# Performance work log

Measured on AMD Instinct MI355X. Metric: run time of the kernel, lower is better.

The kernel has to match this reference:

```python
import jax, jax.numpy as jnp
import numpy as np

N_NODES = 50000
N_EDGES = 800000


def setup_inputs() -> dict:
    key = jax.random.key(0)
    ks = jax.random.split(key, 8)
    x = jax.random.normal(ks[0], (N_NODES, 128), dtype=jnp.float32)
    edge_index = jax.random.randint(ks[1], (2, N_EDGES), 0, N_NODES, dtype=jnp.int64)
    # GCNConv weights (PyG: x @ W then propagate, bias after aggregation)
    W1 = jax.random.normal(ks[2], (128, 256), dtype=jnp.float32) / np.sqrt(128)
    b1 = jnp.zeros((256,), dtype=jnp.float32)
    W2 = jax.random.normal(ks[3], (256, 128), dtype=jnp.float32) / np.sqrt(256)
    b2 = jnp.zeros((128,), dtype=jnp.float32)
    # projection head
    fcW1 = jax.random.normal(ks[4], (128, 128), dtype=jnp.float32) / np.sqrt(128)
    fcb1 = jnp.zeros((128,), dtype=jnp.float32)
    fcW2 = jax.random.normal(ks[5], (128, 128), dtype=jnp.float32) / np.sqrt(128)
    fcb2 = jnp.zeros((128,), dtype=jnp.float32)
    return {"x": x, "edge_index": edge_index, "W1": W1, "b1": b1,
            "W2": W2, "b2": b2, "fcW1": fcW1, "fcb1": fcb1,
            "fcW2": fcW2, "fcb2": fcb2}


def _gcn_conv(x, W, b, src, dst, dinv):
    # x' = D^-1/2 (A + I) D^-1/2 (x W) + b  (GCN with self-loops)
    xw = x @ W                                             # [N, C]
    coeff = dinv[src] * dinv[dst]                          # [E]
    msg = xw[src] * coeff[:, None]                         # [E, C] gather
    agg = jax.ops.segment_sum(msg, dst, num_segments=N_NODES)  # scatter-add
    self_term = xw * (dinv * dinv)[:, None]                # self-loop
    return agg + self_term + b


def reference(x, edge_index, W1, b1, W2, b2, fcW1, fcb1, fcW2, fcb2):
    src, dst = edge_index[0], edge_index[1]
    # degree of A + I (in-degree on dst, weight 1 each, +1 self-loop)
    deg = jax.ops.segment_sum(jnp.ones((N_EDGES,), jnp.float32), dst,
                              num_segments=N_NODES) + 1.0
    dinv = jax.lax.rsqrt(deg)
    # Encoder: GCNConv -> relu -> GCNConv -> relu
    h = jax.nn.relu(_gcn_conv(x, W1, b1, src, dst, dinv))
    z = jax.nn.relu(_gcn_conv(h, W2, b2, src, dst, dinv))
    # projection: Linear -> ELU -> Linear
    p = jax.nn.elu(z @ fcW1 + fcb1)
    return p @ fcW2 + fcb2
```

## Files before the change

### kernel.cpp

```cpp
#include <hip/hip_runtime.h>
#include <hip/hip_bf16.h>
#include <cstdint>

#define N_NODES 50000
#define N_EDGES 800000
#define C128 128
#define SCAN_BLOCKS ((N_NODES + 255) / 256)

typedef __attribute__((ext_vector_type(8))) short bf16x8;
typedef __attribute__((ext_vector_type(4))) float f32x4;
typedef unsigned int u32;
typedef unsigned short u16;

__device__ __forceinline__ bf16x8 pack_bf16x8(u32 a, u32 b, u32 c, u32 d) {
    union { u32 u[4]; bf16x8 v; } x;
    x.u[0] = a; x.u[1] = b; x.u[2] = c; x.u[3] = d;
    return x.v;
}

__device__ __forceinline__ bf16x8 as_bf16x8(uint4 v) {
    union { uint4 u; bf16x8 b; } x;
    x.u = v;
    return x.b;
}

__device__ __forceinline__ u32 rne_bf16(float x) {
    u32 u = __float_as_uint(x);
    return (u + 0x7FFFu + ((u >> 16) & 1u)) >> 16;
}

__device__ __forceinline__ void stage16(const u32* g, u32* lds) {
    __builtin_amdgcn_global_load_lds(
        (const __attribute__((address_space(1))) u32*)g,
        (__attribute__((address_space(3))) u32*)lds, 16, 0, 0);
}


__global__ void k_zero(int* __restrict__ a, int n) {
    int i = blockIdx.x * blockDim.x + threadIdx.x;
    if (i < n) a[i] = 0;
}

__global__ void k_copy(const int* __restrict__ src, int* __restrict__ dst, int n) {
    int i = blockIdx.x * blockDim.x + threadIdx.x;
    if (i < n) dst[i] = src[i];
}

__device__ __forceinline__ int clamp_node(int v) {
    return v < 0 ? 0 : (v >= N_NODES ? N_NODES - 1 : v);
}

__global__ void k_count(const int* __restrict__ ei, int* __restrict__ counts) {
    int e = blockIdx.x * blockDim.x + threadIdx.x;
    if (e < N_EDGES) {
        int dst = clamp_node(ei[N_EDGES + e]);
        atomicAdd(&counts[dst], 1);
    }
}

__global__ void k_dinv(const int* __restrict__ counts, float* __restrict__ dinv) {
    int i = blockIdx.x * blockDim.x + threadIdx.x;
    if (i < N_NODES) {
        dinv[i] = rsqrtf((float)counts[i] + 1.0f);
    }
}

__global__ __launch_bounds__(256) void k_xscale(const float* __restrict__ x,
                                                const float* __restrict__ dinv,
                                                u32* __restrict__ xs ) {
    int idx = blockIdx.x * 256 + threadIdx.x;
    if (idx < N_NODES * 32) {
        int node = idx >> 5;
        float di = dinv[node];
        float4 v = reinterpret_cast<const float4*>(x)[idx];
        u32 w0 = rne_bf16(v.x * di) | (rne_bf16(v.y * di) << 16);
        u32 w1 = rne_bf16(v.z * di) | (rne_bf16(v.w * di) << 16);
        reinterpret_cast<uint2*>(xs)[idx] = make_uint2(w0, w1);
    }
}

__global__ __launch_bounds__(256) void k_scan1(const int* __restrict__ counts,
                                               int* __restrict__ part,
                                               int* __restrict__ bsum) {
    __shared__ int s[256];
    const int tid = threadIdx.x;
    const int i = blockIdx.x * 256 + tid;
    int v = (i < N_NODES) ? counts[i] : 0;
    s[tid] = v;
    __syncthreads();
    for (int off = 1; off < 256; off <<= 1) {
        int t = (tid >= off) ? s[tid - off] : 0;
        __syncthreads();
        s[tid] += t;
        __syncthreads();
    }
    if (i < N_NODES) part[i] = s[tid];
    if (tid == 255) bsum[blockIdx.x] = s[255];
}

__global__ __launch_bounds__(256) void k_scan2(const int* __restrict__ bsum,
                                               int* __restrict__ boff) {
    __shared__ int s[256];
    const int tid = threadIdx.x;
    int v = (tid < SCAN_BLOCKS) ? bsum[tid] : 0;
    s[tid] = v;
    __syncthreads();
    for (int off = 1; off < 256; off <<= 1) {
        int t = (tid >= off) ? s[tid - off] : 0;
        __syncthreads();
        s[tid] += t;
        __syncthreads();
    }
    if (tid < SCAN_BLOCKS) boff[tid] = s[tid] - v;
}

__global__ __launch_bounds__(256) void k_scan3(const int* __restrict__ part,
                                               const int* __restrict__ counts,
                                               const int* __restrict__ boff,
                                               int* __restrict__ offsets) {
    const int i = blockIdx.x * 256 + threadIdx.x;
    if (i < N_NODES) offsets[i] = part[i] - counts[i] + boff[blockIdx.x];
    if (i == 0) offsets[N_NODES] = N_EDGES;
}

__global__ void k_fill(const int* __restrict__ ei, int* __restrict__ cursor,
                       u16* __restrict__ csr) {
    int e = blockIdx.x * blockDim.x + threadIdx.x;
    if (e < N_EDGES) {
        int src = clamp_node(ei[e]);
        int dst = clamp_node(ei[N_EDGES + e]);
        int slot = atomicAdd(&cursor[dst], 1);
        if (slot >= 0 && slot < N_EDGES) csr[slot] = (u16)src;
    }
}


__global__ __launch_bounds__(64) void k_prep(const float* __restrict__ W1,
                                             const float* __restrict__ W2,
                                             const float* __restrict__ fcW1,
                                             const float* __restrict__ fcW2,
                                             u32* __restrict__ ftab) {
    int bx = blockIdx.x;
    int s = bx >> 5, f = bx & 31;
    int kf = f >> 3, nf = f & 7;
    int l = threadIdx.x;
    const float* src; int ld, roff, coff;
    switch (s) {
        case 0:  src = W1;   ld = 256; roff = 0;   coff = 0;   break;
        case 1:  src = W1;   ld = 256; roff = 0;   coff = 128; break;
        case 2:  src = W2;   ld = 128; roff = 0;   coff = 0;   break;
        case 3:  src = W2;   ld = 128; roff = 128; coff = 0;   break;
        case 4:  src = fcW1; ld = 128; roff = 0;   coff = 0;   break;
        default: src = fcW2; ld = 128; roff = 0;   coff = 0;   break;
    }
    int col = coff + nf * 16 + (l & 15);
    int krow = roff + kf * 32 + (l >> 4) * 8;
    u32 hp[4];
#pragma unroll
    for (int p = 0; p < 4; ++p) {
        float a0 = src[(size_t)(krow + 2 * p) * ld + col];
        float a1 = src[(size_t)(krow + 2 * p + 1) * ld + col];
        hp[p] = rne_bf16(a0) | (rne_bf16(a1) << 16);
    }
    u32* dst = ftab + (size_t)s * 8192 + (size_t)f * 256;
    *reinterpret_cast<uint4*>(dst + 4 * l) = make_uint4(hp[0], hp[1], hp[2], hp[3]);
}


template <bool HAS_BIAS, bool RELU>
__global__ __launch_bounds__(256) void k_prop(const u32* __restrict__ xs,
                                              float* __restrict__ out,
                                              const float* __restrict__ dinv,
                                              const int* __restrict__ offsets,
                                              const u16* __restrict__ csr,
                                              const float* __restrict__ bias) {
    const int wave = threadIdx.x >> 6;
    const int lane = threadIdx.x & 63;
    const int half = lane >> 5;
    const int lc   = lane & 31;
    const int node = (blockIdx.x * 4 + wave) * 2 + half;
    if (node >= N_NODES) return;

    const uint2* __restrict__ xp = reinterpret_cast<const uint2*>(xs);
    const float di = dinv[node];

    uint2 sv = xp[(size_t)node * 32 + lc];
    float ax = __uint_as_float(sv.x << 16);
    float ay = __uint_as_float(sv.x & 0xFFFF0000u);
    float az = __uint_as_float(sv.y << 16);
    float aw = __uint_as_float(sv.y & 0xFFFF0000u);

    int e = offsets[node];
    const int eend = offsets[node + 1];
    for (; e + 4 <= eend; e += 4) {
        int s0 = csr[e + 0], s1 = csr[e + 1], s2 = csr[e + 2], s3 = csr[e + 3];
        uint2 v0 = xp[(size_t)s0 * 32 + lc];
        uint2 v1 = xp[(size_t)s1 * 32 + lc];
        uint2 v2 = xp[(size_t)s2 * 32 + lc];
        uint2 v3 = xp[(size_t)s3 * 32 + lc];
        ax += __uint_as_float(v0.x << 16);
        ay += __uint_as_float(v0.x & 0xFFFF0000u);
        az += __uint_as_float(v0.y << 16);
        aw += __uint_as_float(v0.y & 0xFFFF0000u);
        ax += __uint_as_float(v1.x << 16);
        ay += __uint_as_float(v1.x & 0xFFFF0000u);
        az += __uint_as_float(v1.y << 16);
        aw += __uint_as_float(v1.y & 0xFFFF0000u);
        ax += __uint_as_float(v2.x << 16);
        ay += __uint_as_float(v2.x & 0xFFFF0000u);
        az += __uint_as_float(v2.y << 16);
        aw += __uint_as_float(v2.y & 0xFFFF0000u);
        ax += __uint_as_float(v3.x << 16);
        ay += __uint_as_float(v3.x & 0xFFFF0000u);
        az += __uint_as_float(v3.y << 16);
        aw += __uint_as_float(v3.y & 0xFFFF0000u);
    }
    for (; e < eend; ++e) {
        int s = csr[e];
        uint2 v = xp[(size_t)s * 32 + lc];
        ax += __uint_as_float(v.x << 16);
        ay += __uint_as_float(v.x & 0xFFFF0000u);
        az += __uint_as_float(v.y << 16);
        aw += __uint_as_float(v.y & 0xFFFF0000u);
    }

    float4 o;
    o.x = di * ax; o.y = di * ay; o.z = di * az; o.w = di * aw;
    if (HAS_BIAS) {
        float4 bb = reinterpret_cast<const float4*>(bias)[lc];
        o.x += bb.x; o.y += bb.y; o.z += bb.z; o.w += bb.w;
    }
    if (RELU) {
        o.x = fmaxf(o.x, 0.0f); o.y = fmaxf(o.y, 0.0f);
        o.z = fmaxf(o.z, 0.0f); o.w = fmaxf(o.w, 0.0f);
    }
    reinterpret_cast<float4*>(out)[(size_t)node * 32 + lc] = o;
}


template <int NHALF, int ACT1, bool FINAL_BIAS, bool BF16_OUT>
__global__ __launch_bounds__(256, 3) void k_fused(
        const float* __restrict__ A,
        const u32* __restrict__ ftabW1,
        const u32* __restrict__ ftabW2,
        const float* __restrict__ b1v,
        const float* __restrict__ b2v,
        float* __restrict__ C,
        u32* __restrict__ C16,
        const float* __restrict__ dscale,
        int M) {
    __shared__ u32 lds_w[8192];

    const int tid = threadIdx.x;
    const int wave = tid >> 6, l = tid & 63;
    const int l15 = l & 15, l4 = l >> 4;
    const int r = blockIdx.x * 64 + wave * 16 + l15;
    const float* arow = A + (size_t)(r < M ? r : M - 1) * 128;

    auto stage_sec = [&](const u32* sec) {
#pragma unroll
        for (int i = 0; i < 8; ++i) {
            int off = (i * 4 + wave) * 256;
            stage16(sec + off + 4 * l, lds_w + off);
        }
    };

    bf16x8 ahi[4], alo[4];
#pragma unroll
    for (int kf = 0; kf < 4; ++kf) {
        const float* ap = arow + kf * 32 + l4 * 8;
        float4 v0 = *reinterpret_cast<const float4*>(ap);
        float4 v1 = *reinterpret_cast<const float4*>(ap + 4);
        float av[8] = {v0.x, v0.y, v0.z, v0.w, v1.x, v1.y, v1.z, v1.w};
        u32 hp[4], lp[4];
#pragma unroll
        for (int p = 0; p < 4; ++p) {
            float a0 = av[2 * p], a1 = av[2 * p + 1];
            u32 h0 = __float_as_uint(a0) & 0xFFFF0000u;
            u32 h1 = __float_as_uint(a1) & 0xFFFF0000u;
            float q0 = a0 - __uint_as_float(h0);
            float q1 = a1 - __uint_as_float(h1);
            hp[p] = (h0 >> 16) | h1;
            lp[p] = ((__float_as_uint(q0) & 0xFFFF0000u) >> 16) |
                    (__float_as_uint(q1) & 0xFFFF0000u);
        }
        ahi[kf] = pack_bf16x8(hp[0], hp[1], hp[2], hp[3]);
        alo[kf] = pack_bf16x8(lp[0], lp[1], lp[2], lp[3]);
    }

    f32x4 accQ[8] = {};

    stage_sec(ftabW1);
    __syncthreads();

    for (int half = 0; half < NHALF; ++half) {
        f32x4 accH[8] = {};
#pragma unroll
        for (int kf = 0; kf < 4; ++kf) {
            uint4 wh[8];
#pragma unroll
            for (int nf = 0; nf < 8; ++nf)
                wh[nf] = *reinterpret_cast<const uint4*>(
                    lds_w + (kf * 8 + nf) * 256 + 4 * l);
            __builtin_amdgcn_sched_group_barrier(0x100, 8, 0);
#pragma unroll
            for (int nf = 0; nf < 8; ++nf) {
                bf16x8 whi = as_bf16x8(wh[nf]);
                accH[nf] = __builtin_amdgcn_mfma_f32_16x16x32_bf16(whi, ahi[kf], accH[nf], 0, 0, 0);
                accH[nf] = __builtin_amdgcn_mfma_f32_16x16x32_bf16(whi, alo[kf], accH[nf], 0, 0, 0);
            }
            __builtin_amdgcn_sched_group_barrier(0x8, 16, 0);
        }
        __syncthreads();
        stage_sec(ftabW2 + (size_t)half * 8192);

        u32 hpk[8][4];
#pragma unroll
        for (int nf = 0; nf < 8; ++nf) {
            const float4 bb = *reinterpret_cast<const float4*>(
                b1v + half * 128 + nf * 16 + l4 * 4);
            const float bbv[4] = {bb.x, bb.y, bb.z, bb.w};
#pragma unroll
            for (int reg = 0; reg < 4; ++reg) {
                float v = accH[nf][reg] + bbv[reg];
                if (ACT1 == 1) v = fmaxf(v, 0.0f);
                else           v = v > 0.0f ? v : (expf(v) - 1.0f);
                u32 vh = __float_as_uint(v) & 0xFFFF0000u;
                float rr = v - __uint_as_float(vh);
                hpk[nf][reg] = (vh >> 16) | (__float_as_uint(rr) & 0xFFFF0000u);
            }
        }
        __syncthreads();

#pragma unroll
        for (int kf = 0; kf < 4; ++kf) {
            uint4 wh[8];
#pragma unroll
            for (int nf = 0; nf < 8; ++nf)
                wh[nf] = *reinterpret_cast<const uint4*>(
                    lds_w + (kf * 8 + nf) * 256 + 4 * l);
            __builtin_amdgcn_sched_group_barrier(0x100, 8, 0);

            u32 got[8];
#pragma unroll
            for (int je = 0; je < 8; ++je) {
                int srcLane = ((l4 & 1) * 2 + (je >> 2)) * 16 + l15;
                u32 g0 = __shfl(hpk[2 * kf][je & 3], srcLane, 64);
                u32 g1 = __shfl(hpk[2 * kf + 1][je & 3], srcLane, 64);
                got[je] = (l4 & 2) ? g1 : g0;
            }
            u32 hh[4], gg[4];
#pragma unroll
            for (int p = 0; p < 4; ++p) {
                hh[p] = (got[2 * p] & 0xFFFFu) | (got[2 * p + 1] << 16);
                gg[p] = (got[2 * p] >> 16) | (got[2 * p + 1] & 0xFFFF0000u);
            }
            bf16x8 bh = pack_bf16x8(hh[0], hh[1], hh[2], hh[3]);
            bf16x8 bl = pack_bf16x8(gg[0], gg[1], gg[2], gg[3]);

#pragma unroll
            for (int nf = 0; nf < 8; ++nf) {
                bf16x8 whi = as_bf16x8(wh[nf]);
                accQ[nf] = __builtin_amdgcn_mfma_f32_16x16x32_bf16(whi, bh, accQ[nf], 0, 0, 0);
                accQ[nf] = __builtin_amdgcn_mfma_f32_16x16x32_bf16(whi, bl, accQ[nf], 0, 0, 0);
            }
            __builtin_amdgcn_sched_group_barrier(0x8, 16, 0);
        }

        if (half + 1 < NHALF) {
            __syncthreads();
            stage_sec(ftabW1 + (size_t)(half + 1) * 8192);
            __syncthreads();
        }
    }

    if (r < M) {
        if (BF16_OUT) {
            float sc = dscale[r];
#pragma unroll
            for (int nf = 0; nf < 8; ++nf) {
                u32 w0 = rne_bf16(accQ[nf][0] * sc) | (rne_bf16(accQ[nf][1] * sc) << 16);
                u32 w1 = rne_bf16(accQ[nf][2] * sc) | (rne_bf16(accQ[nf][3] * sc) << 16);
                reinterpret_cast<uint2*>(C16)[(size_t)r * 32 + nf * 4 + l4] =
                    make_uint2(w0, w1);
            }
        } else {
#pragma unroll
            for (int nf = 0; nf < 8; ++nf) {
                float4 v;
                v.x = accQ[nf][0]; v.y = accQ[nf][1];
                v.z = accQ[nf][2]; v.w = accQ[nf][3];
                if (FINAL_BIAS) {
                    const float4 bb = *reinterpret_cast<const float4*>(b2v + nf * 16 + l4 * 4);
                    v.x += bb.x; v.y += bb.y; v.z += bb.z; v.w += bb.w;
                }
                *reinterpret_cast<float4*>(C + (size_t)r * 128 + nf * 16 + l4 * 4) = v;
            }
        }
    }
}


extern "C" void kernel_launch(void* const* d_in, const int* in_sizes, int n_in,
                              void* d_out, int out_size, void* d_ws, size_t ws_size,
                              hipStream_t stream) {
    const float* x    = (const float*)d_in[0];
    const int*   ei   = (const int*)d_in[1];
    const float* W1   = (const float*)d_in[2];
    const float* b1   = (const float*)d_in[3];
    const float* W2   = (const float*)d_in[4];
    const float* b2   = (const float*)d_in[5];
    const float* fcW1 = (const float*)d_in[6];
    const float* fcb1 = (const float*)d_in[7];
    const float* fcW2 = (const float*)d_in[8];
    const float* fcb2 = (const float*)d_in[9];
    float* out        = (float*)d_out;

    char* ws = (char*)d_ws;
    size_t off = 0;
    auto alloc = [&](size_t bytes) {
        void* p = ws + off;
        off += (bytes + 255) & ~(size_t)255;
        return p;
    };
    int*   counts  = (int*)alloc(N_NODES * sizeof(int));
    int*   cursor  = (int*)alloc(N_NODES * sizeof(int));
    int*   part    = (int*)alloc(N_NODES * sizeof(int));
    int*   bsum    = (int*)alloc(SCAN_BLOCKS * sizeof(int));
    int*   boff    = (int*)alloc(SCAN_BLOCKS * sizeof(int));
    int*   offsets = (int*)alloc((N_NODES + 1) * sizeof(int));
    u16*   csr     = (u16*)alloc(N_EDGES * sizeof(u16));
    float* dinv    = (float*)alloc(N_NODES * sizeof(float));
    u32*   ftab    = (u32*)alloc((size_t)6 * 8192 * sizeof(u32));
    u32*   xs      = (u32*)alloc((size_t)N_NODES * 128 * 2);
    u32*   qs      = (u32*)alloc((size_t)N_NODES * 128 * 2);
    (void)ws_size; (void)n_in; (void)in_sizes; (void)out_size;

    const u32 SEC = 8192;

    k_zero<<<(N_NODES + 255) / 256, 256, 0, stream>>>(counts, N_NODES);
    k_prep<<<192, 64, 0, stream>>>(W1, W2, fcW1, fcW2, ftab);
    k_count<<<(N_EDGES + 255) / 256, 256, 0, stream>>>(ei, counts);
    k_dinv<<<(N_NODES + 255) / 256, 256, 0, stream>>>(counts, dinv);
    k_xscale<<<(N_NODES * 32 + 255) / 256, 256, 0, stream>>>(x, dinv, xs);
    k_scan1<<<SCAN_BLOCKS, 256, 0, stream>>>(counts, part, bsum);
    k_scan2<<<1, 256, 0, stream>>>(bsum, boff);
    k_scan3<<<SCAN_BLOCKS, 256, 0, stream>>>(part, counts, boff, offsets);
    k_copy<<<(N_NODES + 255) / 256, 256, 0, stream>>>(offsets, cursor, N_NODES);
    k_fill<<<(N_EDGES + 255) / 256, 256, 0, stream>>>(ei, cursor, csr);

    const int prop_grid = (N_NODES + 7) / 8;
    const int gm = (N_NODES + 63) / 64;

    k_prop<false, false><<<prop_grid, 256, 0, stream>>>(xs, out, dinv, offsets, csr, nullptr);

    k_fused<2, 1, false, true><<<gm, 256, 0, stream>>>(out, ftab, ftab + 2 * SEC,
                                                       b1, nullptr, nullptr, qs, dinv, N_NODES);

    k_prop<true, true><<<prop_grid, 256, 0, stream>>>(qs, out, dinv, offsets, csr, b2);

    k_fused<1, 2, true, false><<<gm, 256, 0, stream>>>(out, ftab + 4 * SEC, ftab + 5 * SEC,
                                                       fcb1, fcb2, out, nullptr, nullptr, N_NODES);
}
```

Before: 220.2 us.

## Fuse CSR neighbor aggregation into the MFMA GEMM kernels, drop separate prop kernels

Removes the two standalone k_prop gather kernels and performs the neighbor sum directly inside k_fused, where each lane gathers bf16 rows and accumulates the operand in registers before the MFMA stage. This removes the fp32 intermediate write and re-read of the aggregated features, along with two kernel launches. The cost is that the gather now runs in the GEMM layout: each node's row is handled by 4 lanes with 16-byte loads and no unrolling. Per-lane edge loops diverge within a wave, and the 4 lanes per row scatter their accesses, which may hurt memory-level parallelism compared with the dedicated 32-lanes-per-node gather. Weight staging is moved earlier so it overlaps the gather.

```diff
diff --git a/kernel.cpp b/kernel.cpp
--- a/kernel.cpp
+++ b/kernel.cpp
@@ -4,7 +4,6 @@
 
 #define N_NODES 50000
 #define N_EDGES 800000
-#define C128 128
 #define SCAN_BLOCKS ((N_NODES + 255) / 256)
 
 typedef __attribute__((ext_vector_type(8))) short bf16x8;
@@ -28,6 +27,9 @@
     u32 u = __float_as_uint(x);
     return (u + 0x7FFFu + ((u >> 16) & 1u)) >> 16;
 }
+
+__device__ __forceinline__ float bf16lo(u32 u) { return __uint_as_float(u << 16); }
+__device__ __forceinline__ float bf16hi(u32 u) { return __uint_as_float(u & 0xFFFF0000u); }
 
 __device__ __forceinline__ void stage16(const u32* g, u32* lds) {
     __builtin_amdgcn_global_load_lds(
@@ -67,7 +69,7 @@
 
 __global__ __launch_bounds__(256) void k_xscale(const float* __restrict__ x,
                                                 const float* __restrict__ dinv,
-                                                u32* __restrict__ xs ) {
+                                                u32* __restrict__ xs) {
     int idx = blockIdx.x * 256 + threadIdx.x;
     if (idx < N_NODES * 32) {
         int node = idx >> 5;
@@ -167,87 +169,19 @@
 }
 
 
-template <bool HAS_BIAS, bool RELU>
-__global__ __launch_bounds__(256) void k_prop(const u32* __restrict__ xs,
-                                              float* __restrict__ out,
-                                              const float* __restrict__ dinv,
-                                              const int* __restrict__ offsets,
-                                              const u16* __restrict__ csr,
-                                              const float* __restrict__ bias) {
-    const int wave = threadIdx.x >> 6;
-    const int lane = threadIdx.x & 63;
-    const int half = lane >> 5;
-    const int lc   = lane & 31;
-    const int node = (blockIdx.x * 4 + wave) * 2 + half;
-    if (node >= N_NODES) return;
-
-    const uint2* __restrict__ xp = reinterpret_cast<const uint2*>(xs);
-    const float di = dinv[node];
-
-    uint2 sv = xp[(size_t)node * 32 + lc];
-    float ax = __uint_as_float(sv.x << 16);
-    float ay = __uint_as_float(sv.x & 0xFFFF0000u);
-    float az = __uint_as_float(sv.y << 16);
-    float aw = __uint_as_float(sv.y & 0xFFFF0000u);
-
-    int e = offsets[node];
-    const int eend = offsets[node + 1];
-    for (; e + 4 <= eend; e += 4) {
-        int s0 = csr[e + 0], s1 = csr[e + 1], s2 = csr[e + 2], s3 = csr[e + 3];
-        uint2 v0 = xp[(size_t)s0 * 32 + lc];
-        uint2 v1 = xp[(size_t)s1 * 32 + lc];
-        uint2 v2 = xp[(size_t)s2 * 32 + lc];
-        uint2 v3 = xp[(size_t)s3 * 32 + lc];
-        ax += __uint_as_float(v0.x << 16);
-        ay += __uint_as_float(v0.x & 0xFFFF0000u);
-        az += __uint_as_float(v0.y << 16);
-        aw += __uint_as_float(v0.y & 0xFFFF0000u);
-        ax += __uint_as_float(v1.x << 16);
-        ay += __uint_as_float(v1.x & 0xFFFF0000u);
-        az += __uint_as_float(v1.y << 16);
-        aw += __uint_as_float(v1.y & 0xFFFF0000u);
-        ax += __uint_as_float(v2.x << 16);
-        ay += __uint_as_float(v2.x & 0xFFFF0000u);
-        az += __uint_as_float(v2.y << 16);
-        aw += __uint_as_float(v2.y & 0xFFFF0000u);
-        ax += __uint_as_float(v3.x << 16);
-        ay += __uint_as_float(v3.x & 0xFFFF0000u);
-        az += __uint_as_float(v3.y << 16);
-        aw += __uint_as_float(v3.y & 0xFFFF0000u);
-    }
-    for (; e < eend; ++e) {
-        int s = csr[e];
-        uint2 v = xp[(size_t)s * 32 + lc];
-        ax += __uint_as_float(v.x << 16);
-        ay += __uint_as_float(v.x & 0xFFFF0000u);
-        az += __uint_as_float(v.y << 16);
-        aw += __uint_as_float(v.y & 0xFFFF0000u);
-    }
-
-    float4 o;
-    o.x = di * ax; o.y = di * ay; o.z = di * az; o.w = di * aw;
-    if (HAS_BIAS) {
-        float4 bb = reinterpret_cast<const float4*>(bias)[lc];
-        o.x += bb.x; o.y += bb.y; o.z += bb.z; o.w += bb.w;
-    }
-    if (RELU) {
-        o.x = fmaxf(o.x, 0.0f); o.y = fmaxf(o.y, 0.0f);
-        o.z = fmaxf(o.z, 0.0f); o.w = fmaxf(o.w, 0.0f);
-    }
-    reinterpret_cast<float4*>(out)[(size_t)node * 32 + lc] = o;
-}
-
-
-template <int NHALF, int ACT1, bool FINAL_BIAS, bool BF16_OUT>
+template <int NHALF, int ACT1, bool FINAL_BIAS, bool BF16_OUT, bool GBIAS_RELU>
 __global__ __launch_bounds__(256, 3) void k_fused(
-        const float* __restrict__ A,
+        const u32* __restrict__ Axs,
         const u32* __restrict__ ftabW1,
         const u32* __restrict__ ftabW2,
         const float* __restrict__ b1v,
         const float* __restrict__ b2v,
+        const float* __restrict__ gbias,
         float* __restrict__ C,
         u32* __restrict__ C16,
-        const float* __restrict__ dscale,
+        const float* __restrict__ dinv,
+        const int* __restrict__ offsets,
+        const u16* __restrict__ csr,
         int M) {
     __shared__ u32 lds_w[8192];
 
@@ -255,7 +189,7 @@
     const int wave = tid >> 6, l = tid & 63;
     const int l15 = l & 15, l4 = l >> 4;
     const int r = blockIdx.x * 64 + wave * 16 + l15;
-    const float* arow = A + (size_t)(r < M ? r : M - 1) * 128;
+    const int rc = r < M ? r : M - 1;
 
     auto stage_sec = [&](const u32* sec) {
 #pragma unroll
@@ -265,17 +199,46 @@
         }
     };
 
+    stage_sec(ftabW1);
+
+    float sum[4][8] = {};
+    {
+        auto add_row = [&](int s) {
+            const uint4* rp = reinterpret_cast<const uint4*>(Axs + (size_t)s * 64);
+#pragma unroll
+            for (int kf = 0; kf < 4; ++kf) {
+                uint4 w = rp[kf * 4 + l4];
+                sum[kf][0] += bf16lo(w.x); sum[kf][1] += bf16hi(w.x);
+                sum[kf][2] += bf16lo(w.y); sum[kf][3] += bf16hi(w.y);
+                sum[kf][4] += bf16lo(w.z); sum[kf][5] += bf16hi(w.z);
+                sum[kf][6] += bf16lo(w.w); sum[kf][7] += bf16hi(w.w);
+            }
+        };
+        add_row(rc);
+        const int e1 = offsets[rc + 1];
+        for (int e = offsets[rc]; e < e1; ++e) add_row((int)csr[e]);
+    }
+
+    const float di = dinv[rc];
     bf16x8 ahi[4], alo[4];
 #pragma unroll
     for (int kf = 0; kf < 4; ++kf) {
-        const float* ap = arow + kf * 32 + l4 * 8;
-        float4 v0 = *reinterpret_cast<const float4*>(ap);
-        float4 v1 = *reinterpret_cast<const float4*>(ap + 4);
-        float av[8] = {v0.x, v0.y, v0.z, v0.w, v1.x, v1.y, v1.z, v1.w};
+        float gb[8] = {};
+        if (GBIAS_RELU) {
+            float4 g0 = *reinterpret_cast<const float4*>(gbias + kf * 32 + l4 * 8);
+            float4 g1 = *reinterpret_cast<const float4*>(gbias + kf * 32 + l4 * 8 + 4);
+            gb[0] = g0.x; gb[1] = g0.y; gb[2] = g0.z; gb[3] = g0.w;
+            gb[4] = g1.x; gb[5] = g1.y; gb[6] = g1.z; gb[7] = g1.w;
+        }
         u32 hp[4], lp[4];
 #pragma unroll
         for (int p = 0; p < 4; ++p) {
-            float a0 = av[2 * p], a1 = av[2 * p + 1];
+            float a0 = di * sum[kf][2 * p];
+            float a1 = di * sum[kf][2 * p + 1];
+            if (GBIAS_RELU) {
+                a0 = fmaxf(a0 + gb[2 * p], 0.0f);
+                a1 = fmaxf(a1 + gb[2 * p + 1], 0.0f);
+            }
             u32 h0 = __float_as_uint(a0) & 0xFFFF0000u;
             u32 h1 = __float_as_uint(a1) & 0xFFFF0000u;
             float q0 = a0 - __uint_as_float(h0);
@@ -289,8 +252,6 @@
     }
 
     f32x4 accQ[8] = {};
-
-    stage_sec(ftabW1);
     __syncthreads();
 
     for (int half = 0; half < NHALF; ++half) {
@@ -376,7 +337,7 @@
 
     if (r < M) {
         if (BF16_OUT) {
-            float sc = dscale[r];
+            float sc = dinv[r];
 #pragma unroll
             for (int nf = 0; nf < 8; ++nf) {
                 u32 w0 = rne_bf16(accQ[nf][0] * sc) | (rne_bf16(accQ[nf][1] * sc) << 16);
@@ -449,16 +410,13 @@
     k_copy<<<(N_NODES + 255) / 256, 256, 0, stream>>>(offsets, cursor, N_NODES);
     k_fill<<<(N_EDGES + 255) / 256, 256, 0, stream>>>(ei, cursor, csr);
 
-    const int prop_grid = (N_NODES + 7) / 8;
     const int gm = (N_NODES + 63) / 64;
 
-    k_prop<false, false><<<prop_grid, 256, 0, stream>>>(xs, out, dinv, offsets, csr, nullptr);
-
-    k_fused<2, 1, false, true><<<gm, 256, 0, stream>>>(out, ftab, ftab + 2 * SEC,
-                                                       b1, nullptr, nullptr, qs, dinv, N_NODES);
-
-    k_prop<true, true><<<prop_grid, 256, 0, stream>>>(qs, out, dinv, offsets, csr, b2);
-
-    k_fused<1, 2, true, false><<<gm, 256, 0, stream>>>(out, ftab + 4 * SEC, ftab + 5 * SEC,
-                                                       fcb1, fcb2, out, nullptr, nullptr, N_NODES);
-}
+    k_fused<2, 1, false, true, false><<<gm, 256, 0, stream>>>(
+        xs, ftab, ftab + 2 * SEC, b1, nullptr, nullptr,
+        nullptr, qs, dinv, offsets, csr, N_NODES);
+
+    k_fused<1, 2, true, false, true><<<gm, 256, 0, stream>>>(
+        qs, ftab + 4 * SEC, ftab + 5 * SEC, fcb1, fcb2, b2,
+        out, nullptr, dinv, offsets, csr, N_NODES);
+}
```

Result: slower. 234.4 us (+6.5%).
